# Kernel tuning notes

Hardware: AMD Instinct MI355X
Metric: run time of the kernel (lower is better)

Reference implementation:

```python
import jax, jax.numpy as jnp
import numpy as np

B, T, D, H, A = 1, 262144, 8, 64, 4  # batch, seq_len, state_dim, hidden, n_actions


def setup_inputs() -> dict:
    key = jax.random.key(0)
    ks = jax.random.split(key, 10)
    s = lambda k, shape, sc: jax.random.normal(k, shape, dtype=jnp.float32) * sc
    return {
        "x": jax.random.normal(ks[0], (B, T, D), dtype=jnp.float32),
        # encoder MLP (Dense->tanh, Dense->tanh)
        "W1": s(ks[1], (D, H), 0.5), "b1": jnp.zeros((H,), jnp.float32),
        "W2": s(ks[2], (H, H), 0.15), "b2": jnp.zeros((H,), jnp.float32),
        # SimpleRNN params: h_t = tanh(x_t @ Wx + h_{t-1} @ Wh + b_rnn)
        "Wx": s(ks[3], (H, H), 0.15), "Wh": s(ks[4], (H, H), 0.1),
        "b_rnn": jnp.zeros((H,), jnp.float32),
        # means head
        "Wm": s(ks[5], (H, A), 0.01), "bm": jnp.zeros((A,), jnp.float32),
    }


def reference(x, W1, b1, W2, b2, Wx, Wh, b_rnn, Wm, bm):
    # Masking(mask_value=0): a timestep is masked if ALL features == 0
    mask = jnp.any(x != 0.0, axis=-1)  # [B, T] bool
    # TimeDistributed encoder (applies pointwise over time -> plain batched matmul)
    h1 = jnp.tanh(x @ W1 + b1)          # [B, T, H]
    h2 = jnp.tanh(h1 @ W2 + b2)         # [B, T, H]
    # Precompute input contribution to the RNN outside the scan (efficient form)
    xz = h2 @ Wx + b_rnn                # [B, T, H]

    def step(h, inp):
        z, m = inp                       # z: [B, H], m: [B]
        h_new = jnp.tanh(z + h @ Wh)
        # masked timesteps: carry previous state through (Keras RNN masking semantics)
        h = jnp.where(m[:, None], h_new, h)
        return h, h

    h0 = jnp.zeros((B, H), x.dtype)
    _, hs = jax.lax.scan(step, h0, (jnp.swapaxes(xz, 0, 1), jnp.swapaxes(mask, 0, 1)))
    hs = jnp.swapaxes(hs, 0, 1)          # [B, T, H]
    means = hs @ Wm + bm                 # [B, T, A]
    return means
```

## Files before the change

### kernel.cpp

```cpp
#include <hip/hip_runtime.h>
#include <hip/hip_bf16.h>

constexpr int T_LEN  = 262144;
constexpr int H      = 64;
constexpr int S_LEN  = 8;
constexpr int WARM   = 16;
constexpr int CHUNKS = T_LEN / S_LEN;
constexpr int NWAVE  = CHUNKS / 16;
constexpr int PRE_STRIDE = 68;
constexpr int ZPAD_TAIL = 4;

typedef __attribute__((ext_vector_type(8))) short short8;
typedef __attribute__((ext_vector_type(4))) float f32x4;

__device__ __forceinline__ float fast_tanh(float x) {
    float e = __expf(2.0f * x);
    return 1.0f - 2.0f * __builtin_amdgcn_rcpf(e + 1.0f);
}
__device__ __forceinline__ unsigned short f2bf(float v) {
    unsigned u = __builtin_bit_cast(unsigned, v);
    return (unsigned short)((u + 0x7fffu + ((u >> 16) & 1u)) >> 16);
}
__device__ __forceinline__ float bf2f(unsigned short b) {
    return __builtin_bit_cast(float, (unsigned)b << 16);
}
__device__ __forceinline__ unsigned pack2(float a, float b) {
#if __has_builtin(__builtin_amdgcn_cvt_pk_bf16_f32)
    typedef __attribute__((ext_vector_type(2))) __bf16 bf16x2;
    bf16x2 r = __builtin_amdgcn_cvt_pk_bf16_f32(a, b);
    return __builtin_bit_cast(unsigned, r);
#else
    return (unsigned)f2bf(a) | ((unsigned)f2bf(b) << 16);
#endif
}

__global__ __launch_bounds__(256) void encoder_kernel(
    const float* __restrict__ x,
    const float* __restrict__ W1, const float* __restrict__ b1,
    const float* __restrict__ W2, const float* __restrict__ b2,
    const float* __restrict__ Wx, const float* __restrict__ b_rnn,
    unsigned short* __restrict__ z_s, float* __restrict__ m_s)
{
    __shared__ uint4 w1f[4 * 64];
    __shared__ uint4 w2f[8 * 64];
    __shared__ uint4 w3f[8 * 64];
    __shared__ float pre_[4][16 * PRE_STRIDE];

    const int tid = threadIdx.x;
    const int w   = tid >> 6;
    const int l   = tid & 63;
    const int q   = l >> 4;
    const int l15 = l & 15;

    {
        const int n  = l;
        const int kg = w;
        float v2[16], v3[16];
        #pragma unroll
        for (int kk = 0; kk < 16; ++kk) {
            v2[kk] = W2[(kg * 16 + kk) * 64 + n];
            v3[kk] = Wx[(kg * 16 + kk) * 64 + n];
        }
        const int kh = kg >> 1;
        const int tn = n >> 4;
        #pragma unroll
        for (int s = 0; s < 2; ++s) {
            const int qq   = (2 * kg + s) & 3;
            const int lane = qq * 16 + (n & 15);
            uint4 o2, o3;
            o2.x = pack2(v2[s*8+0], v2[s*8+1]); o2.y = pack2(v2[s*8+2], v2[s*8+3]);
            o2.z = pack2(v2[s*8+4], v2[s*8+5]); o2.w = pack2(v2[s*8+6], v2[s*8+7]);
            o3.x = pack2(v3[s*8+0], v3[s*8+1]); o3.y = pack2(v3[s*8+2], v3[s*8+3]);
            o3.z = pack2(v3[s*8+4], v3[s*8+5]); o3.w = pack2(v3[s*8+6], v3[s*8+7]);
            w2f[(tn * 2 + kh) * 64 + lane] = o2;
            w3f[(tn * 2 + kh) * 64 + lane] = o3;
        }
        uint4 o1 = make_uint4(0, 0, 0, 0);
        if (q < 2) {
            float v1[8];
            #pragma unroll
            for (int j = 0; j < 8; ++j) v1[j] = W1[j * 64 + w * 16 + l15];
            o1.x = pack2(v1[0], v1[1]); o1.y = pack2(v1[2], v1[3]);
            o1.z = pack2(v1[4], v1[5]); o1.w = pack2(v1[6], v1[7]);
        }
        w1f[w * 64 + l] = o1;
    }
    __syncthreads();

    float b1v[4], b2v[4], brv[4];
    #pragma unroll
    for (int tn = 0; tn < 4; ++tn) {
        b1v[tn] = b1[tn * 16 + l15];
        b2v[tn] = b2[tn * 16 + l15];
        brv[tn] = b_rnn[tn * 16 + l15];
    }

    float* mypre = pre_[w];

    float4 xa = make_float4(0.f, 0.f, 0.f, 0.f), xb = xa;
    if (q < 2) {
        const size_t t0 = (size_t)(blockIdx.x * 256 + w * 16 + l15) * 8;
        xa = *(const float4*)(x + t0);
        xb = *(const float4*)(x + t0 + 4);
    }

    #pragma unroll
    for (int it = 0; it < 4; ++it) {
        const int t0w = blockIdx.x * 256 + it * 64 + w * 16;

        float4 na = xa, nb = xb;
        if (it < 3 && q < 2) {
            const size_t tn0 = (size_t)(t0w + 64 + l15) * 8;
            na = *(const float4*)(x + tn0);
            nb = *(const float4*)(x + tn0 + 4);
        }

        short8 a1 = (short8)0;
        if (q < 2) {
            const float xv[8] = {xa.x, xa.y, xa.z, xa.w, xb.x, xb.y, xb.z, xb.w};
            if (q == 0) {
                bool nz = false;
                #pragma unroll
                for (int d = 0; d < 8; ++d) nz = nz || (xv[d] != 0.0f);
                m_s[t0w + l15] = nz ? 1.0f : 0.0f;
                uint4 o;
                o.x = pack2(xv[0], xv[1]); o.y = pack2(xv[2], xv[3]);
                o.z = pack2(xv[4], xv[5]); o.w = pack2(xv[6], xv[7]);
                a1 = __builtin_bit_cast(short8, o);
            } else {
                float lo[8];
                #pragma unroll
                for (int d = 0; d < 8; ++d) lo[d] = xv[d] - bf2f(f2bf(xv[d]));
                uint4 o;
                o.x = pack2(lo[0], lo[1]); o.y = pack2(lo[2], lo[3]);
                o.z = pack2(lo[4], lo[5]); o.w = pack2(lo[6], lo[7]);
                a1 = __builtin_bit_cast(short8, o);
            }
        }

        {
            f32x4 acc[4];
            #pragma unroll
            for (int tn = 0; tn < 4; ++tn)
                acc[tn] = __builtin_amdgcn_mfma_f32_16x16x32_bf16(
                    a1, __builtin_bit_cast(short8, w1f[tn * 64 + l]),
                    (f32x4){0.f, 0.f, 0.f, 0.f}, 0, 0, 0);
            #pragma unroll
            for (int tn = 0; tn < 4; ++tn)
                #pragma unroll
                for (int r = 0; r < 4; ++r)
                    mypre[(q * 4 + r) * PRE_STRIDE + tn * 16 + l15] =
                        fast_tanh(acc[tn][r] + b1v[tn]);
        }
        __builtin_amdgcn_wave_barrier();

        short8 af[2];
        #pragma unroll
        for (int kh = 0; kh < 2; ++kh) {
            const uint4 r0 = *(const uint4*)(mypre + l15 * PRE_STRIDE + kh * 32 + q * 8);
            const uint4 r1 = *(const uint4*)(mypre + l15 * PRE_STRIDE + kh * 32 + q * 8 + 4);
            uint4 p;
            p.x = pack2(__builtin_bit_cast(float, r0.x), __builtin_bit_cast(float, r0.y));
            p.y = pack2(__builtin_bit_cast(float, r0.z), __builtin_bit_cast(float, r0.w));
            p.z = pack2(__builtin_bit_cast(float, r1.x), __builtin_bit_cast(float, r1.y));
            p.w = pack2(__builtin_bit_cast(float, r1.z), __builtin_bit_cast(float, r1.w));
            af[kh] = __builtin_bit_cast(short8, p);
        }
        __builtin_amdgcn_wave_barrier();

        {
            f32x4 acc[4];
            #pragma unroll
            for (int tn = 0; tn < 4; ++tn) {
                f32x4 d = {0.f, 0.f, 0.f, 0.f};
                d = __builtin_amdgcn_mfma_f32_16x16x32_bf16(
                        af[0], __builtin_bit_cast(short8, w2f[(tn * 2 + 0) * 64 + l]), d, 0, 0, 0);
                d = __builtin_amdgcn_mfma_f32_16x16x32_bf16(
                        af[1], __builtin_bit_cast(short8, w2f[(tn * 2 + 1) * 64 + l]), d, 0, 0, 0);
                acc[tn] = d;
            }
            #pragma unroll
            for (int tn = 0; tn < 4; ++tn)
                #pragma unroll
                for (int r = 0; r < 4; ++r)
                    mypre[(q * 4 + r) * PRE_STRIDE + tn * 16 + l15] =
                        fast_tanh(acc[tn][r] + b2v[tn]);
        }
        __builtin_amdgcn_wave_barrier();

        #pragma unroll
        for (int kh = 0; kh < 2; ++kh) {
            const uint4 r0 = *(const uint4*)(mypre + l15 * PRE_STRIDE + kh * 32 + q * 8);
            const uint4 r1 = *(const uint4*)(mypre + l15 * PRE_STRIDE + kh * 32 + q * 8 + 4);
            uint4 p;
            p.x = pack2(__builtin_bit_cast(float, r0.x), __builtin_bit_cast(float, r0.y));
            p.y = pack2(__builtin_bit_cast(float, r0.z), __builtin_bit_cast(float, r0.w));
            p.z = pack2(__builtin_bit_cast(float, r1.x), __builtin_bit_cast(float, r1.y));
            p.w = pack2(__builtin_bit_cast(float, r1.z), __builtin_bit_cast(float, r1.w));
            af[kh] = __builtin_bit_cast(short8, p);
        }
        __builtin_amdgcn_wave_barrier();

        {
            f32x4 acc[4];
            #pragma unroll
            for (int tn = 0; tn < 4; ++tn) {
                f32x4 d = {0.f, 0.f, 0.f, 0.f};
                d = __builtin_amdgcn_mfma_f32_16x16x32_bf16(
                        af[0], __builtin_bit_cast(short8, w3f[(tn * 2 + 0) * 64 + l]), d, 0, 0, 0);
                d = __builtin_amdgcn_mfma_f32_16x16x32_bf16(
                        af[1], __builtin_bit_cast(short8, w3f[(tn * 2 + 1) * 64 + l]), d, 0, 0, 0);
                acc[tn] = d;
            }
            #pragma unroll
            for (int tn = 0; tn < 4; ++tn)
                #pragma unroll
                for (int r = 0; r < 4; ++r)
                    mypre[(q * 4 + r) * PRE_STRIDE + tn * 16 + l15] = acc[tn][r] + brv[tn];
        }
        __builtin_amdgcn_wave_barrier();

        {
            const int ot = l >> 2;
            const int fq = l & 3;
            const float* src = mypre + ot * PRE_STRIDE + fq * 16;
            const uint4 r0 = *(const uint4*)(src + 0);
            const uint4 r1 = *(const uint4*)(src + 4);
            const uint4 r2 = *(const uint4*)(src + 8);
            const uint4 r3 = *(const uint4*)(src + 12);
            uint4 o0, o1;
            o0.x = pack2(__builtin_bit_cast(float, r0.x), __builtin_bit_cast(float, r0.y));
            o0.y = pack2(__builtin_bit_cast(float, r0.z), __builtin_bit_cast(float, r0.w));
            o0.z = pack2(__builtin_bit_cast(float, r1.x), __builtin_bit_cast(float, r1.y));
            o0.w = pack2(__builtin_bit_cast(float, r1.z), __builtin_bit_cast(float, r1.w));
            o1.x = pack2(__builtin_bit_cast(float, r2.x), __builtin_bit_cast(float, r2.y));
            o1.y = pack2(__builtin_bit_cast(float, r2.z), __builtin_bit_cast(float, r2.w));
            o1.z = pack2(__builtin_bit_cast(float, r3.x), __builtin_bit_cast(float, r3.y));
            o1.w = pack2(__builtin_bit_cast(float, r3.z), __builtin_bit_cast(float, r3.w));
            uint4* dst = (uint4*)(z_s + (size_t)(t0w + ot) * 64 + fq * 16);
            dst[0] = o0;
            dst[1] = o1;
        }
        __builtin_amdgcn_wave_barrier();

        xa = na; xb = nb;
    }
}

__global__ __launch_bounds__(256) void rnn_kernel(
    const unsigned short* __restrict__ z_pad, const float* __restrict__ m_pad,
    const float* __restrict__ Wh, const float* __restrict__ Wm,
    const float* __restrict__ bm, float* __restrict__ out)
{
    const int tid = threadIdx.x;
    const int w   = tid >> 6;
    const int l   = tid & 63;
    const int q   = l >> 4;
    const int n15 = l & 15;
    const int rw  = blockIdx.x * 4 + w;
    const int c   = rw * 16 + n15;

    short8 afrag[8];
    #pragma unroll
    for (int tn = 0; tn < 4; ++tn) {
        const int prow = 32 * (tn >> 1) + 8 * (n15 >> 2) + 4 * (tn & 1) + (n15 & 3);
        #pragma unroll
        for (int kh = 0; kh < 2; ++kh) {
            short8 s;
            #pragma unroll
            for (int j = 0; j < 8; ++j)
                s[j] = (short)f2bf(Wh[(kh * 32 + q * 8 + j) * 64 + prow]);
            afrag[tn * 2 + kh] = s;
        }
    }
    short8 wmf[2];
    #pragma unroll
    for (int kh = 0; kh < 2; ++kh) {
        short8 s;
        #pragma unroll
        for (int j = 0; j < 8; ++j)
            s[j] = (n15 < 4) ? (short)f2bf(Wm[(kh * 32 + q * 8 + j) * 4 + n15]) : (short)0;
        wmf[kh] = s;
    }
    const float4 bmv = *(const float4*)bm;

    short8 hB[2];
    hB[0] = (short8)0;
    hB[1] = (short8)0;

    const unsigned short* zrow = z_pad + (size_t)c * S_LEN * 64;
    const float*          mrow = m_pad + (size_t)c * S_LEN;
    const int tneg = -(c * S_LEN);

    const int zo0 = 8 * q;
    const int zo1 = 8 * q + 4;
    const int zo2 = 8 * q + 32;
    const int zo3 = 8 * q + 36;

    uint2 zb0[4], zb1[4];
    float mb0, mb1;
    {
        zb0[0] = *(const uint2*)(zrow + zo0);
        zb0[1] = *(const uint2*)(zrow + zo1);
        zb0[2] = *(const uint2*)(zrow + zo2);
        zb0[3] = *(const uint2*)(zrow + zo3);
        zb1[0] = *(const uint2*)(zrow + 64 + zo0);
        zb1[1] = *(const uint2*)(zrow + 64 + zo1);
        zb1[2] = *(const uint2*)(zrow + 64 + zo2);
        zb1[3] = *(const uint2*)(zrow + 64 + zo3);
    }
    mb0 = mrow[0];
    mb1 = mrow[1];
    zrow += 128; mrow += 2;

    auto body = [&](uint2* zbuf, float& mref,
                    const unsigned short* zrl, const float* mrl,
                    int stv, bool means_prev, bool may_reset) {
        if (may_reset && rw == 0) {
            if (stv == tneg) {
                hB[0] = (short8)0; hB[1] = (short8)0;
            }
        }
        f32x4 acc[4];
        #pragma unroll
        for (int mt = 0; mt < 4; ++mt) {
            f32x4 d = {0.f, 0.f, 0.f, 0.f};
            d = __builtin_amdgcn_mfma_f32_16x16x32_bf16(afrag[mt * 2 + 0], hB[0], d, 0, 0, 0);
            d = __builtin_amdgcn_mfma_f32_16x16x32_bf16(afrag[mt * 2 + 1], hB[1], d, 0, 0, 0);
            acc[mt] = d;
        }
        if (means_prev) {
            f32x4 a2 = {0.f, 0.f, 0.f, 0.f};
            a2 = __builtin_amdgcn_mfma_f32_16x16x32_bf16(wmf[0], hB[0], a2, 0, 0, 0);
            a2 = __builtin_amdgcn_mfma_f32_16x16x32_bf16(wmf[1], hB[1], a2, 0, 0, 0);
            if (q == 0) {
                const size_t tp = (size_t)c * S_LEN + (stv - 1);
                *(float4*)(out + tp * 4) =
                    make_float4(a2[0] + bmv.x, a2[1] + bmv.y, a2[2] + bmv.z, a2[3] + bmv.w);
            }
        }
        const bool upd = (mref != 0.0f);
        #pragma unroll
        for (int tn = 0; tn < 4; ++tn) {
            const unsigned short* zp = (const unsigned short*)&zbuf[tn];
            float th[4];
            #pragma unroll
            for (int r = 0; r < 4; ++r)
                th[r] = fast_tanh(acc[tn][r] + bf2f(zp[r]));
            const unsigned w0 = pack2(th[0], th[1]);
            const unsigned w1 = pack2(th[2], th[3]);
            unsigned* hw = (unsigned*)&hB[tn >> 1];
            const int wi = (tn & 1) * 2;
            hw[wi + 0] = upd ? w0 : hw[wi + 0];
            hw[wi + 1] = upd ? w1 : hw[wi + 1];
        }
        zbuf[0] = *(const uint2*)(zrl + zo0);
        zbuf[1] = *(const uint2*)(zrl + zo1);
        zbuf[2] = *(const uint2*)(zrl + zo2);
        zbuf[3] = *(const uint2*)(zrl + zo3);
        mref = mrl[0];
    };

    for (int i = 0; i < WARM / 2; ++i) {
        const int st = -WARM + 2 * i;
        body(zb0, mb0, zrow,      mrow,     st,     false, true);
        body(zb1, mb1, zrow + 64, mrow + 1, st + 1, false, true);
        zrow += 128; mrow += 2;
    }

    #pragma unroll
    for (int st = 0; st < S_LEN; ++st) {
        if ((st & 1) == 0)
            body(zb0, mb0, zrow + st * 64, mrow + st, st, st >= 1, st == 0);
        else
            body(zb1, mb1, zrow + st * 64, mrow + st, st, true, false);
    }

    {
        f32x4 a2 = {0.f, 0.f, 0.f, 0.f};
        a2 = __builtin_amdgcn_mfma_f32_16x16x32_bf16(wmf[0], hB[0], a2, 0, 0, 0);
        a2 = __builtin_amdgcn_mfma_f32_16x16x32_bf16(wmf[1], hB[1], a2, 0, 0, 0);
        if (q == 0) {
            const size_t tp = (size_t)c * S_LEN + (S_LEN - 1);
            *(float4*)(out + tp * 4) =
                make_float4(a2[0] + bmv.x, a2[1] + bmv.y, a2[2] + bmv.z, a2[3] + bmv.w);
        }
    }
}

extern "C" void kernel_launch(void* const* d_in, const int* in_sizes, int n_in,
                              void* d_out, int out_size, void* d_ws, size_t ws_size,
                              hipStream_t stream) {
    const float* x     = (const float*)d_in[0];
    const float* W1    = (const float*)d_in[1];
    const float* b1    = (const float*)d_in[2];
    const float* W2    = (const float*)d_in[3];
    const float* b2    = (const float*)d_in[4];
    const float* Wx    = (const float*)d_in[5];
    const float* Wh    = (const float*)d_in[6];
    const float* b_rnn = (const float*)d_in[7];
    const float* Wm    = (const float*)d_in[8];
    const float* bm    = (const float*)d_in[9];
    float* out = (float*)d_out;

    unsigned short* z_pad = (unsigned short*)d_ws;
    const size_t z_rows   = (size_t)(WARM + T_LEN + ZPAD_TAIL);
    float*          m_pad = (float*)((char*)d_ws + z_rows * H * 2);

    unsigned short* z_s = z_pad + (size_t)WARM * H;
    float*          m_s = m_pad + WARM;

    encoder_kernel<<<T_LEN / 256, 256, 0, stream>>>(x, W1, b1, W2, b2, Wx, b_rnn, z_s, m_s);
    rnn_kernel<<<NWAVE / 4, 256, 0, stream>>>(z_pad, m_pad, Wh, Wm, bm, out);
}
```

Before: 129.9 us.

## Transpose encoder MFMAs to keep activations in registers, drop LDS staging

The encoder now computes the transposed product (weights as the A operand, activations as B). It permutes the weight rows so each MFMA output tile lands directly in the register layout the next MFMA needs as its B input. This removes the per-layer LDS round-trips, the wave barriers and the repacking from shared memory, and lets z be written straight from registers. In exchange, all lanes now load x and the weight permutation is more intricate, so any indexing mistake would corrupt results. Only the encoder kernel changes; the sequential RNN kernel is untouched, which limits the share of total time affected.

```diff
diff --git a/kernel.cpp b/kernel.cpp
--- a/kernel.cpp
+++ b/kernel.cpp
@@ -7,7 +7,6 @@
 constexpr int WARM   = 16;
 constexpr int CHUNKS = T_LEN / S_LEN;
 constexpr int NWAVE  = CHUNKS / 16;
-constexpr int PRE_STRIDE = 68;
 constexpr int ZPAD_TAIL = 4;
 
 typedef __attribute__((ext_vector_type(8))) short short8;
@@ -41,207 +40,175 @@
     const float* __restrict__ Wx, const float* __restrict__ b_rnn,
     unsigned short* __restrict__ z_s, float* __restrict__ m_s)
 {
-    __shared__ uint4 w1f[4 * 64];
-    __shared__ uint4 w2f[8 * 64];
-    __shared__ uint4 w3f[8 * 64];
-    __shared__ float pre_[4][16 * PRE_STRIDE];
+    __shared__ uint4 w1a[4 * 64];
+    __shared__ uint4 w2a[8 * 64];
+    __shared__ uint4 w3a[8 * 64];
 
     const int tid = threadIdx.x;
     const int w   = tid >> 6;
     const int l   = tid & 63;
     const int q   = l >> 4;
-    const int l15 = l & 15;
+    const int n15 = l & 15;
 
     {
-        const int n  = l;
-        const int kg = w;
-        float v2[16], v3[16];
-        #pragma unroll
-        for (int kk = 0; kk < 16; ++kk) {
-            v2[kk] = W2[(kg * 16 + kk) * 64 + n];
-            v3[kk] = Wx[(kg * 16 + kk) * 64 + n];
-        }
-        const int kh = kg >> 1;
-        const int tn = n >> 4;
-        #pragma unroll
-        for (int s = 0; s < 2; ++s) {
-            const int qq   = (2 * kg + s) & 3;
-            const int lane = qq * 16 + (n & 15);
+        const int smt = tid >> 6;
+        const int sl  = tid & 63;
+        const int sq  = sl >> 4;
+        const int sn  = sl & 15;
+        const int prow = 32 * (smt >> 1) + 8 * (sn >> 2) + 4 * (smt & 1) + (sn & 3);
+
+        uint4 o1 = make_uint4(0, 0, 0, 0);
+        if (sq < 2) {
+            float v[8];
+            #pragma unroll
+            for (int j = 0; j < 8; ++j) v[j] = W1[j * 64 + prow];
+            o1.x = pack2(v[0], v[1]); o1.y = pack2(v[2], v[3]);
+            o1.z = pack2(v[4], v[5]); o1.w = pack2(v[6], v[7]);
+        }
+        w1a[smt * 64 + sl] = o1;
+
+        #pragma unroll
+        for (int kh = 0; kh < 2; ++kh) {
+            float v2[8], v3[8];
+            #pragma unroll
+            for (int j = 0; j < 8; ++j) {
+                const int k = kh * 32 + sq * 8 + j;
+                v2[j] = W2[k * 64 + prow];
+                v3[j] = Wx[k * 64 + prow];
+            }
             uint4 o2, o3;
-            o2.x = pack2(v2[s*8+0], v2[s*8+1]); o2.y = pack2(v2[s*8+2], v2[s*8+3]);
-            o2.z = pack2(v2[s*8+4], v2[s*8+5]); o2.w = pack2(v2[s*8+6], v2[s*8+7]);
-            o3.x = pack2(v3[s*8+0], v3[s*8+1]); o3.y = pack2(v3[s*8+2], v3[s*8+3]);
-            o3.z = pack2(v3[s*8+4], v3[s*8+5]); o3.w = pack2(v3[s*8+6], v3[s*8+7]);
-            w2f[(tn * 2 + kh) * 64 + lane] = o2;
-            w3f[(tn * 2 + kh) * 64 + lane] = o3;
-        }
-        uint4 o1 = make_uint4(0, 0, 0, 0);
-        if (q < 2) {
-            float v1[8];
-            #pragma unroll
-            for (int j = 0; j < 8; ++j) v1[j] = W1[j * 64 + w * 16 + l15];
-            o1.x = pack2(v1[0], v1[1]); o1.y = pack2(v1[2], v1[3]);
-            o1.z = pack2(v1[4], v1[5]); o1.w = pack2(v1[6], v1[7]);
-        }
-        w1f[w * 64 + l] = o1;
+            o2.x = pack2(v2[0], v2[1]); o2.y = pack2(v2[2], v2[3]);
+            o2.z = pack2(v2[4], v2[5]); o2.w = pack2(v2[6], v2[7]);
+            o3.x = pack2(v3[0], v3[1]); o3.y = pack2(v3[2], v3[3]);
+            o3.z = pack2(v3[4], v3[5]); o3.w = pack2(v3[6], v3[7]);
+            w2a[(smt * 2 + kh) * 64 + sl] = o2;
+            w3a[(smt * 2 + kh) * 64 + sl] = o3;
+        }
     }
     __syncthreads();
 
-    float b1v[4], b2v[4], brv[4];
-    #pragma unroll
-    for (int tn = 0; tn < 4; ++tn) {
-        b1v[tn] = b1[tn * 16 + l15];
-        b2v[tn] = b2[tn * 16 + l15];
-        brv[tn] = b_rnn[tn * 16 + l15];
-    }
-
-    float* mypre = pre_[w];
-
-    float4 xa = make_float4(0.f, 0.f, 0.f, 0.f), xb = xa;
-    if (q < 2) {
-        const size_t t0 = (size_t)(blockIdx.x * 256 + w * 16 + l15) * 8;
+    f32x4 b1v[4], b2v[4], brv[4];
+    #pragma unroll
+    for (int mt = 0; mt < 4; ++mt) {
+        const int base = 32 * (mt >> 1) + 4 * (mt & 1) + 8 * q;
+        b1v[mt] = *(const f32x4*)(b1 + base);
+        b2v[mt] = *(const f32x4*)(b2 + base);
+        brv[mt] = *(const f32x4*)(b_rnn + base);
+    }
+
+    float4 xa, xb;
+    {
+        const size_t t0 = (size_t)(blockIdx.x * 256 + w * 16 + n15) * 8;
         xa = *(const float4*)(x + t0);
         xb = *(const float4*)(x + t0 + 4);
     }
 
     #pragma unroll
     for (int it = 0; it < 4; ++it) {
-        const int t0w = blockIdx.x * 256 + it * 64 + w * 16;
+        const int t = blockIdx.x * 256 + it * 64 + w * 16 + n15;
 
         float4 na = xa, nb = xb;
-        if (it < 3 && q < 2) {
-            const size_t tn0 = (size_t)(t0w + 64 + l15) * 8;
+        if (it < 3) {
+            const size_t tn0 = (size_t)(t + 64) * 8;
             na = *(const float4*)(x + tn0);
             nb = *(const float4*)(x + tn0 + 4);
         }
 
-        short8 a1 = (short8)0;
-        if (q < 2) {
+        short8 xB = (short8)0;
+        {
             const float xv[8] = {xa.x, xa.y, xa.z, xa.w, xb.x, xb.y, xb.z, xb.w};
             if (q == 0) {
                 bool nz = false;
                 #pragma unroll
                 for (int d = 0; d < 8; ++d) nz = nz || (xv[d] != 0.0f);
-                m_s[t0w + l15] = nz ? 1.0f : 0.0f;
+                m_s[t] = nz ? 1.0f : 0.0f;
                 uint4 o;
                 o.x = pack2(xv[0], xv[1]); o.y = pack2(xv[2], xv[3]);
                 o.z = pack2(xv[4], xv[5]); o.w = pack2(xv[6], xv[7]);
-                a1 = __builtin_bit_cast(short8, o);
-            } else {
+                xB = __builtin_bit_cast(short8, o);
+            } else if (q == 1) {
                 float lo[8];
                 #pragma unroll
                 for (int d = 0; d < 8; ++d) lo[d] = xv[d] - bf2f(f2bf(xv[d]));
                 uint4 o;
                 o.x = pack2(lo[0], lo[1]); o.y = pack2(lo[2], lo[3]);
                 o.z = pack2(lo[4], lo[5]); o.w = pack2(lo[6], lo[7]);
-                a1 = __builtin_bit_cast(short8, o);
-            }
-        }
-
+                xB = __builtin_bit_cast(short8, o);
+            }
+        }
+
+        f32x4 acc[4];
+        #pragma unroll
+        for (int mt = 0; mt < 4; ++mt)
+            acc[mt] = __builtin_amdgcn_mfma_f32_16x16x32_bf16(
+                __builtin_bit_cast(short8, w1a[mt * 64 + l]), xB,
+                (f32x4){0.f, 0.f, 0.f, 0.f}, 0, 0, 0);
+
+        short8 hb0, hb1;
         {
-            f32x4 acc[4];
-            #pragma unroll
-            for (int tn = 0; tn < 4; ++tn)
-                acc[tn] = __builtin_amdgcn_mfma_f32_16x16x32_bf16(
-                    a1, __builtin_bit_cast(short8, w1f[tn * 64 + l]),
-                    (f32x4){0.f, 0.f, 0.f, 0.f}, 0, 0, 0);
-            #pragma unroll
-            for (int tn = 0; tn < 4; ++tn)
+            unsigned hw[8];
+            #pragma unroll
+            for (int mt = 0; mt < 4; ++mt) {
+                float th[4];
                 #pragma unroll
                 for (int r = 0; r < 4; ++r)
-                    mypre[(q * 4 + r) * PRE_STRIDE + tn * 16 + l15] =
-                        fast_tanh(acc[tn][r] + b1v[tn]);
-        }
-        __builtin_amdgcn_wave_barrier();
-
-        short8 af[2];
-        #pragma unroll
-        for (int kh = 0; kh < 2; ++kh) {
-            const uint4 r0 = *(const uint4*)(mypre + l15 * PRE_STRIDE + kh * 32 + q * 8);
-            const uint4 r1 = *(const uint4*)(mypre + l15 * PRE_STRIDE + kh * 32 + q * 8 + 4);
-            uint4 p;
-            p.x = pack2(__builtin_bit_cast(float, r0.x), __builtin_bit_cast(float, r0.y));
-            p.y = pack2(__builtin_bit_cast(float, r0.z), __builtin_bit_cast(float, r0.w));
-            p.z = pack2(__builtin_bit_cast(float, r1.x), __builtin_bit_cast(float, r1.y));
-            p.w = pack2(__builtin_bit_cast(float, r1.z), __builtin_bit_cast(float, r1.w));
-            af[kh] = __builtin_bit_cast(short8, p);
-        }
-        __builtin_amdgcn_wave_barrier();
-
+                    th[r] = fast_tanh(acc[mt][r] + b1v[mt][r]);
+                hw[mt * 2 + 0] = pack2(th[0], th[1]);
+                hw[mt * 2 + 1] = pack2(th[2], th[3]);
+            }
+            hb0 = __builtin_bit_cast(short8, make_uint4(hw[0], hw[1], hw[2], hw[3]));
+            hb1 = __builtin_bit_cast(short8, make_uint4(hw[4], hw[5], hw[6], hw[7]));
+        }
+
+        #pragma unroll
+        for (int mt = 0; mt < 4; ++mt) {
+            f32x4 d = {0.f, 0.f, 0.f, 0.f};
+            d = __builtin_amdgcn_mfma_f32_16x16x32_bf16(
+                    __builtin_bit_cast(short8, w2a[(mt * 2 + 0) * 64 + l]), hb0, d, 0, 0, 0);
+            d = __builtin_amdgcn_mfma_f32_16x16x32_bf16(
+                    __builtin_bit_cast(short8, w2a[(mt * 2 + 1) * 64 + l]), hb1, d, 0, 0, 0);
+            acc[mt] = d;
+        }
         {
-            f32x4 acc[4];
-            #pragma unroll
-            for (int tn = 0; tn < 4; ++tn) {
-                f32x4 d = {0.f, 0.f, 0.f, 0.f};
-                d = __builtin_amdgcn_mfma_f32_16x16x32_bf16(
-                        af[0], __builtin_bit_cast(short8, w2f[(tn * 2 + 0) * 64 + l]), d, 0, 0, 0);
-                d = __builtin_amdgcn_mfma_f32_16x16x32_bf16(
-                        af[1], __builtin_bit_cast(short8, w2f[(tn * 2 + 1) * 64 + l]), d, 0, 0, 0);
-                acc[tn] = d;
-            }
-            #pragma unroll
-            for (int tn = 0; tn < 4; ++tn)
+            unsigned hw[8];
+            #pragma unroll
+            for (int mt = 0; mt < 4; ++mt) {
+                float th[4];
                 #pragma unroll
                 for (int r = 0; r < 4; ++r)
-                    mypre[(q * 4 + r) * PRE_STRIDE + tn * 16 + l15] =
-                        fast_tanh(acc[tn][r] + b2v[tn]);
-        }
-        __builtin_amdgcn_wave_barrier();
-
-        #pragma unroll
-        for (int kh = 0; kh < 2; ++kh) {
-            const uint4 r0 = *(const uint4*)(mypre + l15 * PRE_STRIDE + kh * 32 + q * 8);
-            const uint4 r1 = *(const uint4*)(mypre + l15 * PRE_STRIDE + kh * 32 + q * 8 + 4);
-            uint4 p;
-            p.x = pack2(__builtin_bit_cast(float, r0.x), __builtin_bit_cast(float, r0.y));
-            p.y = pack2(__builtin_bit_cast(float, r0.z), __builtin_bit_cast(float, r0.w));
-            p.z = pack2(__builtin_bit_cast(float, r1.x), __builtin_bit_cast(float, r1.y));
-            p.w = pack2(__builtin_bit_cast(float, r1.z), __builtin_bit_cast(float, r1.w));
-            af[kh] = __builtin_bit_cast(short8, p);
-        }
-        __builtin_amdgcn_wave_barrier();
+                    th[r] = fast_tanh(acc[mt][r] + b2v[mt][r]);
+                hw[mt * 2 + 0] = pack2(th[0], th[1]);
+                hw[mt * 2 + 1] = pack2(th[2], th[3]);
+            }
+            hb0 = __builtin_bit_cast(short8, make_uint4(hw[0], hw[1], hw[2], hw[3]));
+            hb1 = __builtin_bit_cast(short8, make_uint4(hw[4], hw[5], hw[6], hw[7]));
+        }
+
+        #pragma unroll
+        for (int mt = 0; mt < 4; ++mt) {
+            f32x4 d = {0.f, 0.f, 0.f, 0.f};
+            d = __builtin_amdgcn_mfma_f32_16x16x32_bf16(
+                    __builtin_bit_cast(short8, w3a[(mt * 2 + 0) * 64 + l]), hb0, d, 0, 0, 0);
+            d = __builtin_amdgcn_mfma_f32_16x16x32_bf16(
+                    __builtin_bit_cast(short8, w3a[(mt * 2 + 1) * 64 + l]), hb1, d, 0, 0, 0);
+            acc[mt] = d;
+        }
 
         {
-            f32x4 acc[4];
-            #pragma unroll
-            for (int tn = 0; tn < 4; ++tn) {
-                f32x4 d = {0.f, 0.f, 0.f, 0.f};
-                d = __builtin_amdgcn_mfma_f32_16x16x32_bf16(
-                        af[0], __builtin_bit_cast(short8, w3f[(tn * 2 + 0) * 64 + l]), d, 0, 0, 0);
-                d = __builtin_amdgcn_mfma_f32_16x16x32_bf16(
-                        af[1], __builtin_bit_cast(short8, w3f[(tn * 2 + 1) * 64 + l]), d, 0, 0, 0);
-                acc[tn] = d;
-            }
-            #pragma unroll
-            for (int tn = 0; tn < 4; ++tn)
-                #pragma unroll
-                for (int r = 0; r < 4; ++r)
-                    mypre[(q * 4 + r) * PRE_STRIDE + tn * 16 + l15] = acc[tn][r] + brv[tn];
-        }
-        __builtin_amdgcn_wave_barrier();
-
-        {
-            const int ot = l >> 2;
-            const int fq = l & 3;
-            const float* src = mypre + ot * PRE_STRIDE + fq * 16;
-            const uint4 r0 = *(const uint4*)(src + 0);
-            const uint4 r1 = *(const uint4*)(src + 4);
-            const uint4 r2 = *(const uint4*)(src + 8);
-            const uint4 r3 = *(const uint4*)(src + 12);
-            uint4 o0, o1;
-            o0.x = pack2(__builtin_bit_cast(float, r0.x), __builtin_bit_cast(float, r0.y));
-            o0.y = pack2(__builtin_bit_cast(float, r0.z), __builtin_bit_cast(float, r0.w));
-            o0.z = pack2(__builtin_bit_cast(float, r1.x), __builtin_bit_cast(float, r1.y));
-            o0.w = pack2(__builtin_bit_cast(float, r1.z), __builtin_bit_cast(float, r1.w));
-            o1.x = pack2(__builtin_bit_cast(float, r2.x), __builtin_bit_cast(float, r2.y));
-            o1.y = pack2(__builtin_bit_cast(float, r2.z), __builtin_bit_cast(float, r2.w));
-            o1.z = pack2(__builtin_bit_cast(float, r3.x), __builtin_bit_cast(float, r3.y));
-            o1.w = pack2(__builtin_bit_cast(float, r3.z), __builtin_bit_cast(float, r3.w));
-            uint4* dst = (uint4*)(z_s + (size_t)(t0w + ot) * 64 + fq * 16);
-            dst[0] = o0;
-            dst[1] = o1;
-        }
-        __builtin_amdgcn_wave_barrier();
+            unsigned zw[8];
+            #pragma unroll
+            for (int mt = 0; mt < 4; ++mt) {
+                float z0 = acc[mt][0] + brv[mt][0];
+                float z1 = acc[mt][1] + brv[mt][1];
+                float z2 = acc[mt][2] + brv[mt][2];
+                float z3 = acc[mt][3] + brv[mt][3];
+                zw[mt * 2 + 0] = pack2(z0, z1);
+                zw[mt * 2 + 1] = pack2(z2, z3);
+            }
+            unsigned short* dst = z_s + (size_t)t * 64 + 8 * q;
+            *(uint4*)(dst)      = make_uint4(zw[0], zw[1], zw[2], zw[3]);
+            *(uint4*)(dst + 32) = make_uint4(zw[4], zw[5], zw[6], zw[7]);
+        }
 
         xa = na; xb = nb;
     }
```

New measurement: 128.7 us (median of 2 runs). About the same (-0.9%).
